# Kernel tuning notes

Measured on AMD Instinct MI355X. Metric: run time of the kernel, lower is better.

Reference implementation:

```python
import jax, jax.numpy as jnp
import numpy as np

EPS = 1e-5
SCALE = 30.0

def _ln(x, g, b):
    m = jnp.mean(x, axis=-1, keepdims=True)
    v = jnp.mean((x - m) ** 2, axis=-1, keepdims=True)
    return (x - m) * jax.lax.rsqrt(v + EPS) * g + b

def setup_inputs() -> dict:
    key = jax.random.key(0)
    ks = jax.random.split(key, 12)
    B, L, K, H, NIN = 4, 2048, 48, 128, 512
    s = 0.02
    return {
        "h_V": jax.random.normal(ks[0], (B, L, H), jnp.float32),
        "h_E": jax.random.normal(ks[1], (B, L, K, NIN - H), jnp.float32),
        "mask_V": jnp.ones((B, L), jnp.float32),
        "mask_E": jnp.ones((B, L, K), jnp.float32),
        "w1": jax.random.normal(ks[2], (NIN, H), jnp.float32) * s,
        "b1": jnp.zeros((H,), jnp.float32),
        "w2": jax.random.normal(ks[3], (H, H), jnp.float32) * s,
        "b2": jnp.zeros((H,), jnp.float32),
        "w3": jax.random.normal(ks[4], (H, H), jnp.float32) * s,
        "b3": jnp.zeros((H,), jnp.float32),
        "g1": jnp.ones((H,), jnp.float32),
        "bn1": jnp.zeros((H,), jnp.float32),
        "g2": jnp.ones((H,), jnp.float32),
        "bn2": jnp.zeros((H,), jnp.float32),
        "wf1": jax.random.normal(ks[5], (H, 4 * H), jnp.float32) * s,
        "bf1": jnp.zeros((4 * H,), jnp.float32),
        "wf2": jax.random.normal(ks[6], (4 * H, H), jnp.float32) * s,
        "bf2": jnp.zeros((H,), jnp.float32),
    }

def reference(h_V, h_E, mask_V, mask_E, w1, b1, w2, b2, w3, b3, g1, bn1, g2, bn2, wf1, bf1, wf2, bf2):
    B, L, H = h_V.shape
    K = h_E.shape[-2]
    gelu = lambda x: jax.nn.gelu(x, approximate=False)  # torch nn.GELU default (erf)
    # expand source node over K neighbors and concat: (B,L,K,num_in)
    h_V_exp = jnp.broadcast_to(h_V[:, :, None, :], (B, L, K, H))
    h_EV = jnp.concatenate([h_V_exp, h_E], axis=-1)
    h_msg = gelu(jnp.einsum('blki,ih->blkh', h_EV, w1) + b1)
    h_msg = gelu(jnp.einsum('blkh,hj->blkj', h_msg, w2) + b2)
    h_msg = jnp.einsum('blkh,hj->blkj', h_msg, w3) + b3
    h_msg = mask_E[..., None] * h_msg
    dh = jnp.sum(h_msg, axis=-2) / SCALE  # masked sum-aggregate over K
    h = _ln(h_V + dh, g1, bn1)
    dff = jnp.einsum('blh,hf->blf', h, wf1) + bf1
    dff = jnp.einsum('blf,fh->blh', gelu(dff), wf2) + bf2
    h = _ln(h + dff, g2, bn2)
    return mask_V[..., None] * h
```

## Files before the change

### kernel.cpp

```cpp
#include <hip/hip_runtime.h>
#include <hip/hip_bf16.h>


typedef __bf16 bf16x8 __attribute__((ext_vector_type(8)));
typedef __bf16 bf16x4 __attribute__((ext_vector_type(4)));
typedef float f32x4 __attribute__((ext_vector_type(4)));

#define HH 128
#define EE 384
#define KK 48

__device__ __forceinline__ float gelu_f(float x) {
  float x2 = x * x;
  float u = x * (-1.5957691216f - 0.0713548163f * x2);
  float e = __expf(u);
  return __fdividef(x, 1.0f + e);
}

__device__ __forceinline__ bf16x8 cvt8v(f32x4 a, f32x4 b) {
  bf16x8 r;
  #pragma unroll
  for (int i = 0; i < 4; ++i) { r[i] = (__bf16)a[i]; r[i + 4] = (__bf16)b[i]; }
  return r;
}

__device__ __forceinline__ f32x4 mfma16(bf16x8 a, bf16x8 b, f32x4 c) {
  return __builtin_amdgcn_mfma_f32_16x16x32_bf16(a, b, c, 0, 0, 0);
}

__device__ __forceinline__ void gload16(const void* g, void* l) {
  __builtin_amdgcn_global_load_lds(
      (const __attribute__((address_space(1))) void*)g,
      (__attribute__((address_space(3))) void*)l, 16, 0, 0);
}

__global__ void prep_kernel(const float* __restrict__ w1, const float* __restrict__ w2,
                            const float* __restrict__ w3, const float* __restrict__ wf1,
                            const float* __restrict__ wf2, __bf16* __restrict__ out) {
  int idx = blockIdx.x * 256 + threadIdx.x;
  if (idx < 49152) {
    int t = idx & 7, lane = (idx >> 3) & 63, n = (idx >> 9) & 7, kc = idx >> 12;
    int e = kc * 32 + (lane >> 4) * 8 + t, h = n * 16 + (lane & 15);
    out[idx] = (__bf16)w1[(128 + e) * 128 + h];
  } else if (idx < 65536) {
    int u = idx - 49152;
    int t = u & 7, lane = (u >> 3) & 63, n = (u >> 9) & 7, kc = u >> 12;
    int e = kc * 32 + (lane >> 4) * 8 + t, h = n * 16 + (lane & 15);
    out[idx] = (__bf16)w2[e * 128 + h];
  } else if (idx < 81920) {
    int u = idx - 65536;
    int t = u & 7, lane = (u >> 3) & 63, n = (u >> 9) & 7, kc = u >> 12;
    int e = kc * 32 + (lane >> 4) * 8 + t, h = n * 16 + (lane & 15);
    out[idx] = (__bf16)w3[e * 128 + h];
  } else if (idx < 147456) {
    int t = idx - 81920; int f = t >> 7, h = t & 127;
    out[idx] = (__bf16)wf1[h * 512 + f];
  } else if (idx < 212992) {
    int t = idx - 147456; int h = t >> 9, f = t & 511;
    out[idx] = (__bf16)wf2[f * 128 + h];
  }
}

__global__ __launch_bounds__(128) void v1_kernel(const float* __restrict__ hV,
                                                 const float* __restrict__ w1,
                                                 const float* __restrict__ b1,
                                                 float* __restrict__ V1) {
  __shared__ __align__(16) float sV[16][128];
  const int tid = threadIdx.x;
  const long p0 = (long)blockIdx.x * 16;
  for (int i = 0; i < 16; ++i) sV[i][tid] = hV[(p0 + i) * HH + tid];
  __syncthreads();
  float acc[16];
  float bb = b1[tid];
  #pragma unroll
  for (int p = 0; p < 16; ++p) acc[p] = bb;
  for (int k = 0; k < 128; k += 4) {
    float wa = w1[(k + 0) * HH + tid];
    float wb = w1[(k + 1) * HH + tid];
    float wc = w1[(k + 2) * HH + tid];
    float wd = w1[(k + 3) * HH + tid];
    #pragma unroll
    for (int p = 0; p < 16; ++p) {
      float4 h4 = *(const float4*)&sV[p][k];
      acc[p] = fmaf(h4.x, wa, fmaf(h4.y, wb, fmaf(h4.z, wc, fmaf(h4.w, wd, acc[p]))));
    }
  }
  #pragma unroll
  for (int p = 0; p < 16; ++p) V1[(p0 + p) * HH + tid] = acc[p];
}

__global__ __launch_bounds__(256, 2) void msg_kernel(
    const float* __restrict__ hE, const float* __restrict__ hV,
    const float* __restrict__ maskE,
    const __bf16* __restrict__ w1f, const __bf16* __restrict__ w2f,
    const __bf16* __restrict__ w3f, const float* __restrict__ V1,
    const float* __restrict__ b2, const float* __restrict__ b3,
    const float* __restrict__ g1, const float* __restrict__ bn1,
    float* __restrict__ outH) {
  __shared__ __align__(16) float sStage[4][4608];

  const int tid = threadIdx.x;
  const int lane = tid & 63;
  const int w = tid >> 6;
  const long p = (long)blockIdx.x * 4 + w;
  const int fr = lane & 15;
  const int fg = lane >> 4;
  char* stDst = (char*)&sStage[w][0];
  const int swz = (fr & 7) << 4;

  const int r_l = lane >> 3;
  const int cswz = ((lane & 7) ^ r_l) * 16;
  const char* gA = (const char*)(hE + p * KK * (long)EE) + r_l * (EE * 4) + cswz;

  const __bf16* b1p = w1f + lane * 8;
  const __bf16* b2p = w2f + lane * 8;
  const __bf16* b3p = w3f + lane * 8;

  f32x4 acc[3][8];
  #pragma unroll
  for (int m = 0; m < 3; ++m)
    #pragma unroll
    for (int n = 0; n < 8; ++n) acc[m][n] = (f32x4){0.f, 0.f, 0.f, 0.f};

  bf16x8 BA[8], BB[8], BC[8];

#define STAGEA(KC, BUFI) { \
    _Pragma("unroll") for (int q_ = 0; q_ < 6; ++q_) \
      gload16(gA + (KC) * 128 + q_ * (8 * EE * 4), stDst + (BUFI) * 6144 + q_ * 1024); }
#define LOADB(BUF, BP, KC) { \
    _Pragma("unroll") for (int n_ = 0; n_ < 8; ++n_) \
      BUF[n_] = *(const bf16x8*)((BP) + ((KC) * 8 + n_) * 512); }
#define WAITV(N) asm volatile("s_waitcnt vmcnt(" #N ")" ::: "memory")
#define WAITL   asm volatile("s_waitcnt lgkmcnt(0)" ::: "memory")
#define SBAR    __builtin_amdgcn_sched_barrier(0)

#define GITER(WAITN, BUFI, BUSE, BLD, BLP, BLKC, DOSTAGE, STKC, STBUF) { \
    WAITV(WAITN); \
    const char* rb_ = stDst + (BUFI) * 6144; \
    f32x4 x0_ = *(const f32x4*)(rb_ + fr * 128 + ((fg * 32) ^ swz)); \
    f32x4 x1_ = *(const f32x4*)(rb_ + fr * 128 + ((fg * 32 + 16) ^ swz)); \
    f32x4 x2_ = *(const f32x4*)(rb_ + (16 + fr) * 128 + ((fg * 32) ^ swz)); \
    f32x4 x3_ = *(const f32x4*)(rb_ + (16 + fr) * 128 + ((fg * 32 + 16) ^ swz)); \
    f32x4 x4_ = *(const f32x4*)(rb_ + (32 + fr) * 128 + ((fg * 32) ^ swz)); \
    f32x4 x5_ = *(const f32x4*)(rb_ + (32 + fr) * 128 + ((fg * 32 + 16) ^ swz)); \
    WAITL; SBAR; \
    LOADB(BLD, BLP, BLKC); \
    SBAR; \
    if (DOSTAGE) STAGEA(STKC, STBUF); \
    SBAR; \
    bf16x8 af0 = cvt8v(x0_, x1_); \
    bf16x8 af1 = cvt8v(x2_, x3_); \
    bf16x8 af2 = cvt8v(x4_, x5_); \
    _Pragma("unroll") for (int n_ = 0; n_ < 8; ++n_) { \
      acc[0][n_] = mfma16(BUSE[n_], af0, acc[0][n_]); \
      acc[1][n_] = mfma16(BUSE[n_], af1, acc[1][n_]); \
      acc[2][n_] = mfma16(BUSE[n_], af2, acc[2][n_]); } }

#define STEPL(BUSE, KC) { \
    const int cb_ = (((KC) * 64 + fg * 16) ^ swz); \
    bf16x8 af0 = *(const bf16x8*)(stDst + fr * 256 + cb_); \
    bf16x8 af1 = *(const bf16x8*)(stDst + (16 + fr) * 256 + cb_); \
    bf16x8 af2 = *(const bf16x8*)(stDst + (32 + fr) * 256 + cb_); \
    _Pragma("unroll") for (int n_ = 0; n_ < 8; ++n_) { \
      acc[0][n_] = mfma16(BUSE[n_], af0, acc[0][n_]); \
      acc[1][n_] = mfma16(BUSE[n_], af1, acc[1][n_]); \
      acc[2][n_] = mfma16(BUSE[n_], af2, acc[2][n_]); } }
#define EPI(BIASQ) { \
    _Pragma("unroll") for (int m_ = 0; m_ < 3; ++m_) { \
      const int rb_ = (m_ * 16 + fr) * 256; \
      _Pragma("unroll") for (int n_ = 0; n_ < 8; ++n_) { \
        bf16x4 t_; \
        _Pragma("unroll") for (int j_ = 0; j_ < 4; ++j_) \
          t_[j_] = (__bf16)gelu_f(acc[m_][n_][j_] + BIASQ[n_][j_]); \
        *(bf16x4*)(stDst + rb_ + ((n_ * 32 + fg * 8) ^ swz)) = t_; \
        acc[m_][n_] = (f32x4){0.f, 0.f, 0.f, 0.f}; } } }

  STAGEA(0, 0); SBAR;
  LOADB(BA, b1p, 0); SBAR;
  STAGEA(1, 1); SBAR;
  LOADB(BB, b1p, 1); SBAR;
  STAGEA(2, 2); SBAR;

  GITER(20, 0, BA, BC, b1p, 2, 1, 3, 0);
  GITER(20, 1, BB, BA, b1p, 3, 1, 4, 1);
  GITER(20, 2, BC, BB, b1p, 4, 1, 5, 2);
  GITER(20, 0, BA, BC, b1p, 5, 1, 6, 0);
  GITER(20, 1, BB, BA, b1p, 6, 1, 7, 1);
  GITER(20, 2, BC, BB, b1p, 7, 1, 8, 2);
  GITER(20, 0, BA, BC, b1p, 8, 1, 9, 0);
  GITER(20, 1, BB, BA, b1p, 9, 1, 10, 1);
  GITER(20, 2, BC, BB, b1p, 10, 1, 11, 2);
  GITER(20, 0, BA, BC, b1p, 11, 0, 0, 0);
  GITER(14, 1, BB, BA, b2p, 0, 0, 0, 0);
  GITER(8,  2, BC, BB, b2p, 1, 0, 0, 0);

  {
    f32x4 vq[8];
    #pragma unroll
    for (int n = 0; n < 8; ++n) vq[n] = *(const f32x4*)(V1 + p * HH + n * 16 + fg * 4);
    EPI(vq);
  }

  STEPL(BA, 0); LOADB(BC, b2p, 2);
  STEPL(BB, 1); LOADB(BA, b2p, 3);
  STEPL(BC, 2); LOADB(BB, b3p, 0);
  STEPL(BA, 3); LOADB(BC, b3p, 1);
  {
    f32x4 bq[8];
    #pragma unroll
    for (int n = 0; n < 8; ++n) bq[n] = *(const f32x4*)(b2 + n * 16 + fg * 4);
    EPI(bq);
  }

  STEPL(BB, 0); LOADB(BA, b3p, 2);
  STEPL(BC, 1); LOADB(BB, b3p, 3);
  STEPL(BA, 2);
  STEPL(BB, 3);

  const float mk0 = maskE[p * KK + fr];
  const float mk1 = maskE[p * KK + 16 + fr];
  const float mk2 = maskE[p * KK + 32 + fr];
  f32x4 red[8];
  {
    #pragma unroll
    for (int n = 0; n < 8; ++n) {
      f32x4 bq = *(const f32x4*)(b3 + n * 16 + fg * 4);
      red[n] = mk0 * (acc[0][n] + bq) + mk1 * (acc[1][n] + bq) + mk2 * (acc[2][n] + bq);
    }
    #pragma unroll
    for (int off = 1; off <= 8; off <<= 1)
      #pragma unroll
      for (int n = 0; n < 8; ++n)
        #pragma unroll
        for (int j = 0; j < 4; ++j)
          red[n][j] += __shfl_xor(red[n][j], off);
  }

  {
    f32x4 xq[8];
    #pragma unroll
    for (int n = 0; n < 8; ++n)
      xq[n] = *(const f32x4*)(hV + p * HH + n * 16 + fg * 4) + red[n] * (1.f / 30.f);
    float s = 0.f;
    #pragma unroll
    for (int n = 0; n < 8; ++n)
      #pragma unroll
      for (int j = 0; j < 4; ++j) s += xq[n][j];
    s += __shfl_xor(s, 16); s += __shfl_xor(s, 32);
    float mean = s * (1.f / 128.f);
    float qv = 0.f;
    #pragma unroll
    for (int n = 0; n < 8; ++n)
      #pragma unroll
      for (int j = 0; j < 4; ++j) { float e = xq[n][j] - mean; qv += e * e; }
    qv += __shfl_xor(qv, 16); qv += __shfl_xor(qv, 32);
    float rs = rsqrtf(qv * (1.f / 128.f) + 1e-5f);
    if (fr == 0) {
      #pragma unroll
      for (int n = 0; n < 8; ++n) {
        f32x4 gq = *(const f32x4*)(g1 + n * 16 + fg * 4);
        f32x4 bq = *(const f32x4*)(bn1 + n * 16 + fg * 4);
        f32x4 o;
        #pragma unroll
        for (int j = 0; j < 4; ++j) o[j] = (xq[n][j] - mean) * rs * gq[j] + bq[j];
        *(f32x4*)(outH + p * HH + n * 16 + fg * 4) = o;
      }
    }
  }
#undef STAGEA
#undef LOADB
#undef WAITV
#undef WAITL
#undef SBAR
#undef GITER
#undef STEPL
#undef EPI
}

__global__ __launch_bounds__(256, 2) void ffn_kernel(
    const float* __restrict__ xin, const __bf16* __restrict__ wf1t,
    const float* __restrict__ bf1, const __bf16* __restrict__ wf2t,
    const float* __restrict__ bf2, const float* __restrict__ g2,
    const float* __restrict__ bn2, const float* __restrict__ maskV,
    float* __restrict__ out) {
  __shared__ __align__(16) __bf16 sX[32][136];
  __shared__ __align__(16) __bf16 sH1[32][520];
  __shared__ __align__(16) float sOut[32][132];
  const int tid = threadIdx.x, lane = tid & 63, w = tid >> 6;
  const long row0 = (long)blockIdx.x * 32;
  const int fr = lane & 15, fg = lane >> 4;

  {
    int r = tid >> 3, c = (tid & 7) * 16;
    const float* src = xin + (row0 + r) * HH + c;
    f32x4 v0 = *(const f32x4*)src, v1 = *(const f32x4*)(src + 4);
    f32x4 v2 = *(const f32x4*)(src + 8), v3 = *(const f32x4*)(src + 12);
    *(bf16x8*)&sX[r][c] = cvt8v(v0, v1);
    *(bf16x8*)&sX[r][c + 8] = cvt8v(v2, v3);
  }
  __syncthreads();

  f32x4 a1[2][8];
  #pragma unroll
  for (int m = 0; m < 2; ++m)
    #pragma unroll
    for (int n = 0; n < 8; ++n) a1[m][n] = (f32x4){0.f, 0.f, 0.f, 0.f};
  for (int kc = 0; kc < 4; ++kc) {
    int k0 = kc * 32;
    bf16x8 af0 = *(const bf16x8*)&sX[fr][k0 + fg * 8];
    bf16x8 af1 = *(const bf16x8*)&sX[16 + fr][k0 + fg * 8];
    #pragma unroll
    for (int n = 0; n < 8; ++n) {
      const __bf16* bp = wf1t + (long)(w * 128 + n * 16 + fr) * HH + k0 + fg * 8;
      bf16x8 bfr = *(const bf16x8*)bp;
      a1[0][n] = mfma16(af0, bfr, a1[0][n]);
      a1[1][n] = mfma16(af1, bfr, a1[1][n]);
    }
  }
  #pragma unroll
  for (int n = 0; n < 8; ++n) {
    float bv = bf1[w * 128 + n * 16 + fr];
    #pragma unroll
    for (int m = 0; m < 2; ++m)
      #pragma unroll
      for (int j = 0; j < 4; ++j)
        sH1[m * 16 + fg * 4 + j][w * 128 + n * 16 + fr] = (__bf16)gelu_f(a1[m][n][j] + bv);
  }
  __syncthreads();

  f32x4 a2[2][2];
  #pragma unroll
  for (int m = 0; m < 2; ++m)
    #pragma unroll
    for (int n = 0; n < 2; ++n) a2[m][n] = (f32x4){0.f, 0.f, 0.f, 0.f};
  for (int kc = 0; kc < 16; ++kc) {
    int k0 = kc * 32;
    bf16x8 af0 = *(const bf16x8*)&sH1[fr][k0 + fg * 8];
    bf16x8 af1 = *(const bf16x8*)&sH1[16 + fr][k0 + fg * 8];
    #pragma unroll
    for (int n = 0; n < 2; ++n) {
      const __bf16* bp = wf2t + (long)(w * 32 + n * 16 + fr) * 512 + k0 + fg * 8;
      bf16x8 bfr = *(const bf16x8*)bp;
      a2[0][n] = mfma16(af0, bfr, a2[0][n]);
      a2[1][n] = mfma16(af1, bfr, a2[1][n]);
    }
  }
  #pragma unroll
  for (int n = 0; n < 2; ++n) {
    float bv = bf2[w * 32 + n * 16 + fr];
    #pragma unroll
    for (int m = 0; m < 2; ++m)
      #pragma unroll
      for (int j = 0; j < 4; ++j)
        sOut[m * 16 + fg * 4 + j][w * 32 + n * 16 + fr] = a2[m][n][j] + bv;
  }
  __syncthreads();

  {
    int r = tid >> 3, c0 = (tid & 7) * 16;
    long p = row0 + r;
    const float* xp = xin + p * HH + c0;
    float x[16];
    #pragma unroll
    for (int i = 0; i < 16; ++i) x[i] = xp[i] + sOut[r][c0 + i];
    float s = 0.f;
    #pragma unroll
    for (int i = 0; i < 16; ++i) s += x[i];
    s += __shfl_xor(s, 1); s += __shfl_xor(s, 2); s += __shfl_xor(s, 4);
    float mean = s * (1.f / 128.f);
    float q = 0.f;
    #pragma unroll
    for (int i = 0; i < 16; ++i) { float e = x[i] - mean; q += e * e; }
    q += __shfl_xor(q, 1); q += __shfl_xor(q, 2); q += __shfl_xor(q, 4);
    float rs = rsqrtf(q * (1.f / 128.f) + 1e-5f);
    float mv = maskV[p];
    float* op = out + p * HH + c0;
    #pragma unroll
    for (int i = 0; i < 16; ++i)
      op[i] = ((x[i] - mean) * rs * g2[c0 + i] + bn2[c0 + i]) * mv;
  }
}

extern "C" void kernel_launch(void* const* d_in, const int* in_sizes, int n_in,
                              void* d_out, int out_size, void* d_ws, size_t ws_size,
                              hipStream_t stream) {
  const float* hV    = (const float*)d_in[0];
  const float* hE    = (const float*)d_in[1];
  const float* maskV = (const float*)d_in[2];
  const float* maskE = (const float*)d_in[3];
  const float* w1    = (const float*)d_in[4];
  const float* b1    = (const float*)d_in[5];
  const float* w2    = (const float*)d_in[6];
  const float* b2    = (const float*)d_in[7];
  const float* w3    = (const float*)d_in[8];
  const float* b3    = (const float*)d_in[9];
  const float* g1    = (const float*)d_in[10];
  const float* bn1   = (const float*)d_in[11];
  const float* g2    = (const float*)d_in[12];
  const float* bn2   = (const float*)d_in[13];
  const float* wf1   = (const float*)d_in[14];
  const float* bf1   = (const float*)d_in[15];
  const float* wf2   = (const float*)d_in[16];
  const float* bf2   = (const float*)d_in[17];
  float* out = (float*)d_out;

  __bf16* wsb = (__bf16*)d_ws;
  float* V1   = (float*)((char*)d_ws + 425984);
  float* hbuf = (float*)((char*)d_ws + 4620288);

  prep_kernel<<<832, 256, 0, stream>>>(w1, w2, w3, wf1, wf2, wsb);
  v1_kernel<<<512, 128, 0, stream>>>(hV, w1, b1, V1);
  msg_kernel<<<2048, 256, 0, stream>>>(hE, hV, maskE,
                                       wsb, wsb + 49152, wsb + 65536, V1,
                                       b2, b3, g1, bn1, hbuf);
  ffn_kernel<<<256, 256, 0, stream>>>(hbuf, wsb + 81920, bf1, wsb + 147456, bf2,
                                      g2, bn2, maskV, out);
}
```

Before: 244.6 us.

## Double-buffer weight fragments and reload them after MFMAs to cut registers

Switches from triple-buffered B weight fragments to two register buffers. Each buffer is reloaded right after its MFMA block consumes it, and the A-stage prefetch depth drops from three stages to two. The explicit sched_barriers and lgkmcnt waits are removed, and vmcnt waits are retuned to match. The aim is lower VGPR pressure and better occupancy or scheduling freedom, at the cost of a shallower prefetch and a risk of exposed load latency or miscounted waits.

```diff
diff --git a/kernel.cpp b/kernel.cpp
--- a/kernel.cpp
+++ b/kernel.cpp
@@ -122,7 +122,7 @@
     #pragma unroll
     for (int n = 0; n < 8; ++n) acc[m][n] = (f32x4){0.f, 0.f, 0.f, 0.f};
 
-  bf16x8 BA[8], BB[8], BC[8];
+  bf16x8 BsA[8], BsB[8];
 
 #define STAGEA(KC, BUFI) { \
     _Pragma("unroll") for (int q_ = 0; q_ < 6; ++q_) \
@@ -131,10 +131,8 @@
     _Pragma("unroll") for (int n_ = 0; n_ < 8; ++n_) \
       BUF[n_] = *(const bf16x8*)((BP) + ((KC) * 8 + n_) * 512); }
 #define WAITV(N) asm volatile("s_waitcnt vmcnt(" #N ")" ::: "memory")
-#define WAITL   asm volatile("s_waitcnt lgkmcnt(0)" ::: "memory")
-#define SBAR    __builtin_amdgcn_sched_barrier(0)
-
-#define GITER(WAITN, BUFI, BUSE, BLD, BLP, BLKC, DOSTAGE, STKC, STBUF) { \
+
+#define GITER(WAITN, BUFI, BUSE, DOSTAGE, STKC, STBUF, DOB, BLP, BLKC) { \
     WAITV(WAITN); \
     const char* rb_ = stDst + (BUFI) * 6144; \
     f32x4 x0_ = *(const f32x4*)(rb_ + fr * 128 + ((fg * 32) ^ swz)); \
@@ -143,20 +141,17 @@
     f32x4 x3_ = *(const f32x4*)(rb_ + (16 + fr) * 128 + ((fg * 32 + 16) ^ swz)); \
     f32x4 x4_ = *(const f32x4*)(rb_ + (32 + fr) * 128 + ((fg * 32) ^ swz)); \
     f32x4 x5_ = *(const f32x4*)(rb_ + (32 + fr) * 128 + ((fg * 32 + 16) ^ swz)); \
-    WAITL; SBAR; \
-    LOADB(BLD, BLP, BLKC); \
-    SBAR; \
     if (DOSTAGE) STAGEA(STKC, STBUF); \
-    SBAR; \
     bf16x8 af0 = cvt8v(x0_, x1_); \
     bf16x8 af1 = cvt8v(x2_, x3_); \
     bf16x8 af2 = cvt8v(x4_, x5_); \
     _Pragma("unroll") for (int n_ = 0; n_ < 8; ++n_) { \
       acc[0][n_] = mfma16(BUSE[n_], af0, acc[0][n_]); \
       acc[1][n_] = mfma16(BUSE[n_], af1, acc[1][n_]); \
-      acc[2][n_] = mfma16(BUSE[n_], af2, acc[2][n_]); } }
-
-#define STEPL(BUSE, KC) { \
+      acc[2][n_] = mfma16(BUSE[n_], af2, acc[2][n_]); } \
+    if (DOB) LOADB(BUSE, BLP, BLKC); }
+
+#define STEPL(BUSE, KC, DOB, BLP, BLKC) { \
     const int cb_ = (((KC) * 64 + fg * 16) ^ swz); \
     bf16x8 af0 = *(const bf16x8*)(stDst + fr * 256 + cb_); \
     bf16x8 af1 = *(const bf16x8*)(stDst + (16 + fr) * 256 + cb_); \
@@ -164,7 +159,9 @@
     _Pragma("unroll") for (int n_ = 0; n_ < 8; ++n_) { \
       acc[0][n_] = mfma16(BUSE[n_], af0, acc[0][n_]); \
       acc[1][n_] = mfma16(BUSE[n_], af1, acc[1][n_]); \
-      acc[2][n_] = mfma16(BUSE[n_], af2, acc[2][n_]); } }
+      acc[2][n_] = mfma16(BUSE[n_], af2, acc[2][n_]); } \
+    if (DOB) LOADB(BUSE, BLP, BLKC); }
+
 #define EPI(BIASQ) { \
     _Pragma("unroll") for (int m_ = 0; m_ < 3; ++m_) { \
       const int rb_ = (m_ * 16 + fr) * 256; \
@@ -175,36 +172,35 @@
         *(bf16x4*)(stDst + rb_ + ((n_ * 32 + fg * 8) ^ swz)) = t_; \
         acc[m_][n_] = (f32x4){0.f, 0.f, 0.f, 0.f}; } } }
 
-  STAGEA(0, 0); SBAR;
-  LOADB(BA, b1p, 0); SBAR;
-  STAGEA(1, 1); SBAR;
-  LOADB(BB, b1p, 1); SBAR;
-  STAGEA(2, 2); SBAR;
-
-  GITER(20, 0, BA, BC, b1p, 2, 1, 3, 0);
-  GITER(20, 1, BB, BA, b1p, 3, 1, 4, 1);
-  GITER(20, 2, BC, BB, b1p, 4, 1, 5, 2);
-  GITER(20, 0, BA, BC, b1p, 5, 1, 6, 0);
-  GITER(20, 1, BB, BA, b1p, 6, 1, 7, 1);
-  GITER(20, 2, BC, BB, b1p, 7, 1, 8, 2);
-  GITER(20, 0, BA, BC, b1p, 8, 1, 9, 0);
-  GITER(20, 1, BB, BA, b1p, 9, 1, 10, 1);
-  GITER(20, 2, BC, BB, b1p, 10, 1, 11, 2);
-  GITER(20, 0, BA, BC, b1p, 11, 0, 0, 0);
-  GITER(14, 1, BB, BA, b2p, 0, 0, 0, 0);
-  GITER(8,  2, BC, BB, b2p, 1, 0, 0, 0);
-
-  {
-    f32x4 vq[8];
-    #pragma unroll
-    for (int n = 0; n < 8; ++n) vq[n] = *(const f32x4*)(V1 + p * HH + n * 16 + fg * 4);
-    EPI(vq);
-  }
-
-  STEPL(BA, 0); LOADB(BC, b2p, 2);
-  STEPL(BB, 1); LOADB(BA, b2p, 3);
-  STEPL(BC, 2); LOADB(BB, b3p, 0);
-  STEPL(BA, 3); LOADB(BC, b3p, 1);
+  STAGEA(0, 0);
+  LOADB(BsA, b1p, 0);
+  STAGEA(1, 1);
+  LOADB(BsB, b1p, 1);
+
+  GITER(14, 0, BsA, 1, 2, 2, 1, b1p, 2);
+  GITER(14, 1, BsB, 1, 3, 0, 1, b1p, 3);
+  GITER(14, 2, BsA, 1, 4, 1, 1, b1p, 4);
+  GITER(14, 0, BsB, 1, 5, 2, 1, b1p, 5);
+  GITER(14, 1, BsA, 1, 6, 0, 1, b1p, 6);
+  GITER(14, 2, BsB, 1, 7, 1, 1, b1p, 7);
+  GITER(14, 0, BsA, 1, 8, 2, 1, b1p, 8);
+  GITER(14, 1, BsB, 1, 9, 0, 1, b1p, 9);
+  GITER(14, 2, BsA, 1, 10, 1, 1, b1p, 10);
+  GITER(14, 0, BsB, 1, 11, 2, 1, b1p, 11);
+
+  f32x4 vq[8];
+  #pragma unroll
+  for (int n = 0; n < 8; ++n) vq[n] = *(const f32x4*)(V1 + p * HH + n * 16 + fg * 4);
+
+  GITER(22, 1, BsA, 0, 0, 0, 1, b2p, 0);
+  GITER(16, 2, BsB, 0, 0, 0, 1, b2p, 1);
+
+  EPI(vq);
+
+  { WAITV(8);  STEPL(BsA, 0, 1, b2p, 2); }
+  { WAITV(8);  STEPL(BsB, 1, 1, b2p, 3); }
+  { WAITV(8);  STEPL(BsA, 2, 1, b3p, 0); }
+  { WAITV(8);  STEPL(BsB, 3, 1, b3p, 1); }
   {
     f32x4 bq[8];
     #pragma unroll
@@ -212,10 +208,10 @@
     EPI(bq);
   }
 
-  STEPL(BB, 0); LOADB(BA, b3p, 2);
-  STEPL(BC, 1); LOADB(BB, b3p, 3);
-  STEPL(BA, 2);
-  STEPL(BB, 3);
+  { STEPL(BsA, 0, 1, b3p, 2); }
+  { STEPL(BsB, 1, 1, b3p, 3); }
+  { WAITV(8);  STEPL(BsA, 2, 0, b3p, 0); }
+  { WAITV(0);  STEPL(BsB, 3, 0, b3p, 0); }
 
   const float mk0 = maskE[p * KK + fr];
   const float mk1 = maskE[p * KK + 16 + fr];
@@ -270,8 +266,6 @@
 #undef STAGEA
 #undef LOADB
 #undef WAITV
-#undef WAITL
-#undef SBAR
 #undef GITER
 #undef STEPL
 #undef EPI
```

New measurement: 211.9 us. 1.15x faster.
